# Optimization experiments

Measured on AMD Instinct MI355X. Metric: run time of the kernel, lower is better.

## Reference

```python
import jax, jax.numpy as jnp
import numpy as np

D_MODEL = 1024
D_STATE = 16
D_CONV = 4
EXPAND = 2
D_INNER = D_MODEL * EXPAND


def setup_inputs() -> dict:
    key = jax.random.key(0)
    ks = jax.random.split(key, 8)
    B, L = 2, 2048
    x = jax.random.normal(ks[0], (B, L, D_MODEL), dtype=jnp.float32)
    # in_proj: Linear(d_model -> 2*d_inner), no bias
    W_in = jax.random.normal(ks[1], (D_MODEL, 2 * D_INNER), dtype=jnp.float32) / np.sqrt(D_MODEL)
    # depthwise conv1d: (d_inner, 1, d_conv) + bias
    conv_w = jax.random.normal(ks[2], (D_INNER, 1, D_CONV), dtype=jnp.float32) / np.sqrt(D_CONV)
    conv_b = jax.random.normal(ks[3], (D_INNER,), dtype=jnp.float32) * 0.01
    # x_proj: Linear(d_inner -> 2*d_state + 1), no bias
    W_x = jax.random.normal(ks[4], (D_INNER, 2 * D_STATE + 1), dtype=jnp.float32) / np.sqrt(D_INNER)
    # A_log ~ Uniform(-log(d_state), -1)
    A_log = jax.random.uniform(ks[5], (D_INNER, D_STATE), dtype=jnp.float32,
                               minval=-np.log(D_STATE), maxval=-1.0)
    D_param = jnp.ones((D_INNER,), dtype=jnp.float32)
    W_out = jax.random.normal(ks[6], (D_INNER, D_MODEL), dtype=jnp.float32) / np.sqrt(D_INNER)
    return {"x": x, "W_in": W_in, "conv_w": conv_w, "conv_b": conv_b,
            "W_x": W_x, "A_log": A_log, "D_param": D_param, "W_out": W_out}


def _selective_scan(x, delta, A, Bm, Cm):
    # x:(B,L,D), delta:(B,L), A:(D,N), Bm/Cm:(B,L,N)
    Bsz, L, Dd = x.shape
    N = A.shape[1]
    h0 = jnp.zeros((Bsz, Dd, N), dtype=x.dtype)

    def step(h, inp):
        dt, Bt, Ct, xt = inp  # (B,), wait dt:(B,), Bt:(B,N), Ct:(B,N), xt:(B,D)
        A_bar = jnp.exp(dt[:, None, None] * A)          # (B,D,N)
        dB = (dt[:, None] * Bt)[:, None, :]             # (B,1,N)
        h = A_bar * h + dB * xt[:, :, None]             # (B,D,N)
        y = jnp.einsum('bn,bdn->bd', Ct, h)             # (B,D)
        return h, y

    xs = (jnp.swapaxes(delta, 0, 1), jnp.swapaxes(Bm, 0, 1),
          jnp.swapaxes(Cm, 0, 1), jnp.swapaxes(x, 0, 1))
    _, ys = jax.lax.scan(step, h0, xs)                  # ys: (L,B,D)
    return jnp.swapaxes(ys, 0, 1)


def reference(x, W_in, conv_w, conv_b, W_x, A_log, D_param, W_out):
    B, L, _ = x.shape
    xr = x @ W_in                                       # (B,L,2*Di)
    x_inner, res = jnp.split(xr, 2, axis=-1)
    # causal depthwise conv: left-pad d_conv-1, valid conv == torch slice [:L]
    xc = jnp.swapaxes(x_inner, 1, 2)                    # (B,Di,L)
    xc = jax.lax.conv_general_dilated(
        xc, conv_w, window_strides=(1,), padding=[(D_CONV - 1, 0)],
        dimension_numbers=('NCH', 'OIH', 'NCH'), feature_group_count=D_INNER)
    xc = xc + conv_b[None, :, None]
    xc = jnp.swapaxes(xc, 1, 2)                         # (B,L,Di)
    xc = jax.nn.silu(xc)
    ssm_params = xc @ W_x                               # (B,L,1+2N)
    delta = jax.nn.softplus(ssm_params[..., 0])         # (B,L)
    Bm = ssm_params[..., 1:1 + D_STATE]                 # (B,L,N)
    Cm = ssm_params[..., 1 + D_STATE:]                  # (B,L,N)
    A = -jnp.exp(A_log)                                 # (Di,N)
    y = _selective_scan(xc, delta, A, Bm, Cm)           # (B,L,Di)
    y = y + xc * D_param[None, None, :]
    y = y * jax.nn.silu(res)
    return y @ W_out                                    # (B,L,d_model)
```

## Files before the change

kernel.cpp:

```cpp
#include <hip/hip_runtime.h>

#define L_SEQ 2048
#define NB    2
#define DMOD  1024
#define DIN   2048
#define NST   16
#define NROWS (NB*L_SEQ)
#define CL    64
#define NC    (L_SEQ/CL)

typedef unsigned short u16;
typedef _Float16 half8 __attribute__((ext_vector_type(8)));
typedef float f32x4 __attribute__((ext_vector_type(4)));
typedef short short8 __attribute__((ext_vector_type(8)));

__device__ __forceinline__ float siluf(float v){ return v / (1.f + __expf(-v)); }
__device__ __forceinline__ u16 f2h_bits(float v){ _Float16 h = (_Float16)v; return __builtin_bit_cast(u16, h); }
__device__ __forceinline__ float h2f(u16 v){ return (float)__builtin_bit_cast(_Float16, v); }
__device__ __forceinline__ float fexp2(float x){
#if __has_builtin(__builtin_amdgcn_exp2f)
    return __builtin_amdgcn_exp2f(x);
#else
    return __expf(x * 0.69314718056f);
#endif
}

__device__ __forceinline__ void gload16(const u16* g, u16* l)
{
    __builtin_amdgcn_global_load_lds(
        (const __attribute__((address_space(1))) void*)g,
        (__attribute__((address_space(3))) void*)l,
        16, 0, 0);
}

#define BARRIER() do { asm volatile("" ::: "memory"); __builtin_amdgcn_s_barrier(); asm volatile("" ::: "memory"); } while (0)
#define VMCNT2()  asm volatile("s_waitcnt vmcnt(2)" ::: "memory")

__global__ __launch_bounds__(256)
void prep_inputs(const float* __restrict__ x, const float* __restrict__ W_in,
                 const float* __restrict__ W_out, const float* __restrict__ Wx,
                 u16* __restrict__ x16, u16* __restrict__ Bt1,
                 u16* __restrict__ Bt3, u16* __restrict__ WxT16)
{
    __shared__ float s[64][65];
    const int bid = blockIdx.x, tid = threadIdx.x;
    if (bid < 4096) {
        int i = bid * 256 + tid;
        float4 v = ((const float4*)x)[i];
        ushort4 o;
        o.x = f2h_bits(v.x); o.y = f2h_bits(v.y); o.z = f2h_bits(v.z); o.w = f2h_bits(v.w);
        *(ushort4*)&x16[(size_t)i * 4] = o;
    } else if (bid < 5632) {
        const float* in; u16* outT; int R, C, rblk, cblk;
        if (bid < 5120) { int b = bid - 4096; in = W_in;  outT = Bt1; R = 1024; C = 4096; cblk = b & 63; rblk = b >> 6; }
        else            { int b = bid - 5120; in = W_out; outT = Bt3; R = 2048; C = 1024; cblk = b & 15; rblk = b >> 4; }
        int r0 = rblk * 64, c0 = cblk * 64;
        int tc = tid & 63, ty = tid >> 6;
        #pragma unroll
        for (int j = 0; j < 16; j++) {
            int r = ty + j * 4;
            s[r][tc] = in[(size_t)(r0 + r) * C + c0 + tc];
        }
        __syncthreads();
        #pragma unroll
        for (int j = 0; j < 16; j++) {
            int nn = ty + j * 4;
            outT[(size_t)(c0 + nn) * R + r0 + tc] = f2h_bits(s[tc][nn]);
        }
    } else {
        int idx = (bid - 5632) * 256 + tid;
        int n = idx >> 11, k = idx & 2047;
        float v = (n < 33) ? Wx[k * 33 + n] : 0.f;
        WxT16[idx] = f2h_bits(v);
    }
}

template<int EPI>
__global__ __launch_bounds__(512, 2)
void gemm8(const u16* __restrict__ A, const u16* __restrict__ Bt,
           void* __restrict__ C0v, void* __restrict__ C1v,
           int M, int N, int KLEN, int lda, int ldb)
{
    __shared__ __align__(16) u16 As[2 * 256 * 64];
    __shared__ __align__(16) u16 Bs[2 * 256 * 64];
    const int tid  = threadIdx.x;
    const int lane = tid & 63;
    const int w    = tid >> 6;
    const int wm   = w >> 2, wn = w & 3;
    const int bm = blockIdx.y * 256, bn = blockIdx.x * 256;
    const int kBase = blockIdx.z * KLEN;

    const int srow8 = lane >> 3;
    const int sunit = (lane & 7) ^ srow8;
    const u16* Ag = A  + (size_t)(bm + srow8) * lda + kBase + sunit * 8;
    const u16* Bg = Bt + (size_t)(bn + srow8) * ldb + kBase + sunit * 8;
    const int rw = w * 16;

    const int fr  = lane & 15;
    const int sl0 = ((lane >> 4) ^ (fr & 7)) * 8;
    int aOffs[8], bOffs[4];
    #pragma unroll
    for (int mi = 0; mi < 8; mi++) aOffs[mi] = (wm * 128 + mi * 16 + fr) * 64 + sl0;
    #pragma unroll
    for (int ni = 0; ni < 4; ni++) bOffs[ni] = (ni * 64 + wn * 16 + fr) * 64 + sl0;

    f32x4 acc[8][4];
    #pragma unroll
    for (int i = 0; i < 8; i++)
        #pragma unroll
        for (int j = 0; j < 4; j++)
            acc[i][j] = (f32x4){0.f, 0.f, 0.f, 0.f};

    auto stage2 = [&](const u16* G, int ld, int rbase, int kcol, u16* ldsDst) {
        gload16(G + (size_t)rbase * ld + kcol, ldsDst);
        gload16(G + (size_t)(rbase + 8) * ld + kcol, ldsDst + 8 * 64);
    };

    const int NT = KLEN >> 6;
    stage2(Ag, lda, 0 + rw, 0, &As[(0 + rw) * 64]);
    stage2(Ag, lda, 128 + rw, 0, &As[(128 + rw) * 64]);
    stage2(Bg, ldb, 0 + rw, 0, &Bs[(0 + rw) * 64]);
    stage2(Bg, ldb, 128 + rw, 0, &Bs[(128 + rw) * 64]);
    VMCNT2();
    BARRIER();

    for (int t = 0; t < NT; ++t) {
        const int cO = (t & 1) << 14;
        const int nO = cO ^ 16384;
        const int kn = (t + 1) << 6;
        const bool pf = (t + 1) < NT;
        half8 af[8], bf0, bf1;

        #pragma unroll
        for (int mi = 0; mi < 8; mi++) af[mi] = *(const half8*)&As[cO + aOffs[mi]];
        bf0 = *(const half8*)&Bs[cO + bOffs[0]];
        bf1 = *(const half8*)&Bs[cO + bOffs[1]];
        if (pf) stage2(Ag, lda, 0 + rw, kn, &As[nO + (0 + rw) * 64]);
        BARRIER();
        __builtin_amdgcn_s_setprio(1);
        #pragma unroll
        for (int mi = 0; mi < 8; mi++) acc[mi][0] = __builtin_amdgcn_mfma_f32_16x16x32_f16(af[mi], bf0, acc[mi][0], 0, 0, 0);
        #pragma unroll
        for (int mi = 0; mi < 8; mi++) acc[mi][1] = __builtin_amdgcn_mfma_f32_16x16x32_f16(af[mi], bf1, acc[mi][1], 0, 0, 0);
        __builtin_amdgcn_s_setprio(0);
        VMCNT2();
        BARRIER();

        bf0 = *(const half8*)&Bs[cO + bOffs[2]];
        bf1 = *(const half8*)&Bs[cO + bOffs[3]];
        if (pf) stage2(Ag, lda, 128 + rw, kn, &As[nO + (128 + rw) * 64]);
        BARRIER();
        __builtin_amdgcn_s_setprio(1);
        #pragma unroll
        for (int mi = 0; mi < 8; mi++) acc[mi][2] = __builtin_amdgcn_mfma_f32_16x16x32_f16(af[mi], bf0, acc[mi][2], 0, 0, 0);
        #pragma unroll
        for (int mi = 0; mi < 8; mi++) acc[mi][3] = __builtin_amdgcn_mfma_f32_16x16x32_f16(af[mi], bf1, acc[mi][3], 0, 0, 0);
        __builtin_amdgcn_s_setprio(0);
        BARRIER();

        #pragma unroll
        for (int mi = 0; mi < 8; mi++) af[mi] = *(const half8*)&As[cO + (aOffs[mi] ^ 32)];
        bf0 = *(const half8*)&Bs[cO + (bOffs[0] ^ 32)];
        bf1 = *(const half8*)&Bs[cO + (bOffs[1] ^ 32)];
        if (pf) stage2(Bg, ldb, 0 + rw, kn, &Bs[nO + (0 + rw) * 64]);
        BARRIER();
        __builtin_amdgcn_s_setprio(1);
        #pragma unroll
        for (int mi = 0; mi < 8; mi++) acc[mi][0] = __builtin_amdgcn_mfma_f32_16x16x32_f16(af[mi], bf0, acc[mi][0], 0, 0, 0);
        #pragma unroll
        for (int mi = 0; mi < 8; mi++) acc[mi][1] = __builtin_amdgcn_mfma_f32_16x16x32_f16(af[mi], bf1, acc[mi][1], 0, 0, 0);
        __builtin_amdgcn_s_setprio(0);
        BARRIER();

        bf0 = *(const half8*)&Bs[cO + (bOffs[2] ^ 32)];
        bf1 = *(const half8*)&Bs[cO + (bOffs[3] ^ 32)];
        if (pf) stage2(Bg, ldb, 128 + rw, kn, &Bs[nO + (128 + rw) * 64]);
        BARRIER();
        __builtin_amdgcn_s_setprio(1);
        #pragma unroll
        for (int mi = 0; mi < 8; mi++) acc[mi][2] = __builtin_amdgcn_mfma_f32_16x16x32_f16(af[mi], bf0, acc[mi][2], 0, 0, 0);
        #pragma unroll
        for (int mi = 0; mi < 8; mi++) acc[mi][3] = __builtin_amdgcn_mfma_f32_16x16x32_f16(af[mi], bf1, acc[mi][3], 0, 0, 0);
        __builtin_amdgcn_s_setprio(0);
        VMCNT2();
        BARRIER();
    }

    const int cr = (lane >> 4) * 4;
    #pragma unroll
    for (int mi = 0; mi < 8; mi++) {
        #pragma unroll
        for (int ni = 0; ni < 4; ni++) {
            #pragma unroll
            for (int q = 0; q < 4; q++) {
                int row = bm + wm * 128 + mi * 16 + cr + q;
                int col = bn + ni * 64 + wn * 16 + fr;
                float v = acc[mi][ni][q];
                if (EPI == 1) {
                    int half = N >> 1;
                    if (col < half) ((u16*)C0v)[(size_t)row * half + col] = f2h_bits(v);
                    else            ((u16*)C1v)[(size_t)row * half + col - half] = f2h_bits(siluf(v));
                } else {
                    ((u16*)C0v)[((size_t)blockIdx.z * M + row) * N + col] = f2h_bits(v);
                }
            }
        }
    }
}

__global__ __launch_bounds__(256)
void add_partials4(const u16* __restrict__ p, float* __restrict__ out)
{
    int i = blockIdx.x * 256 + threadIdx.x;
    const size_t stride = (size_t)NROWS * DMOD;
    float acc[8] = {0,0,0,0,0,0,0,0};
    #pragma unroll
    for (int z = 0; z < 4; z++) {
        short8 a = *(const short8*)&p[z * stride + (size_t)i * 8];
        #pragma unroll
        for (int j = 0; j < 8; j++) acc[j] += h2f((u16)a[j]);
    }
    float4 o0 = {acc[0], acc[1], acc[2], acc[3]};
    float4 o1 = {acc[4], acc[5], acc[6], acc[7]};
    *(float4*)&out[(size_t)i * 8]     = o0;
    *(float4*)&out[(size_t)i * 8 + 4] = o1;
}

__global__ __launch_bounds__(256)
void conv_silu16(const u16* __restrict__ xin16, const float* __restrict__ cw,
                 const float* __restrict__ cb, u16* __restrict__ xc16)
{
    int idx = blockIdx.x * 256 + threadIdx.x;
    int d8 = idx & 255;
    int t  = (idx >> 8) & (L_SEQ - 1);
    int b  = idx >> 19;
    int d  = d8 << 3;
    const float4* cw4 = (const float4*)cw;
    float4 w[8];
    #pragma unroll
    for (int j = 0; j < 8; j++) w[j] = cw4[d + j];
    float acc[8];
    {
        float4 b0 = *(const float4*)&cb[d];
        float4 b1 = *(const float4*)&cb[d + 4];
        acc[0]=b0.x; acc[1]=b0.y; acc[2]=b0.z; acc[3]=b0.w;
        acc[4]=b1.x; acc[5]=b1.y; acc[6]=b1.z; acc[7]=b1.w;
    }
    #pragma unroll
    for (int k = 0; k < 4; k++) {
        int tt = t + k - 3;
        if (tt >= 0) {
            short8 v = *(const short8*)&xin16[((size_t)(b * L_SEQ + tt)) * DIN + d];
            #pragma unroll
            for (int j = 0; j < 8; j++)
                acc[j] = fmaf(h2f((u16)v[j]), (&w[j].x)[k], acc[j]);
        }
    }
    short8 o;
    #pragma unroll
    for (int j = 0; j < 8; j++) o[j] = (short)f2h_bits(siluf(acc[j]));
    *(short8*)&xc16[(size_t)idx * 8] = o;
}

__global__ __launch_bounds__(256)
void gemm2_mfma(const u16* __restrict__ A, const u16* __restrict__ Bt, float* __restrict__ pb)
{
    __shared__ __align__(16) u16 As[64 * 64];
    __shared__ __align__(16) u16 Bs[48 * 64];
    const int tid = threadIdx.x, lane = tid & 63, w = tid >> 6;
    const int bm = blockIdx.x * 64;
    const int kz = blockIdx.y;
    const int arow = tid >> 2;
    const int au   = (tid & 3) << 1;
    f32x4 acc[3];
    acc[0] = acc[1] = acc[2] = (f32x4){0.f, 0.f, 0.f, 0.f};

    for (int it = 0; it < 4; ++it) {
        const int k0 = kz * 256 + it * 64;
        short8 ra0 = *(const short8*)&A[(size_t)(bm + arow) * DIN + k0 + au * 8];
        short8 ra1 = *(const short8*)&A[(size_t)(bm + arow) * DIN + k0 + (au + 1) * 8];
        short8 rb0, rb1;
        if (tid < 192) {
            rb0 = *(const short8*)&Bt[(size_t)arow * DIN + k0 + au * 8];
            rb1 = *(const short8*)&Bt[(size_t)arow * DIN + k0 + (au + 1) * 8];
        }
        __syncthreads();
        {
            int s0 = au ^ (arow & 7), s1 = (au + 1) ^ (arow & 7);
            *(short8*)&As[arow * 64 + s0 * 8] = ra0;
            *(short8*)&As[arow * 64 + s1 * 8] = ra1;
            if (tid < 192) {
                *(short8*)&Bs[arow * 64 + s0 * 8] = rb0;
                *(short8*)&Bs[arow * 64 + s1 * 8] = rb1;
            }
        }
        __syncthreads();
        #pragma unroll
        for (int kk = 0; kk < 2; kk++) {
            int r = w * 16 + (lane & 15);
            int sl = (kk * 4 + (lane >> 4)) ^ (r & 7);
            half8 af = *(const half8*)&As[r * 64 + sl * 8];
            #pragma unroll
            for (int ni = 0; ni < 3; ni++) {
                int br = ni * 16 + (lane & 15);
                int bsl = (kk * 4 + (lane >> 4)) ^ (br & 7);
                half8 bf = *(const half8*)&Bs[br * 64 + bsl * 8];
                acc[ni] = __builtin_amdgcn_mfma_f32_16x16x32_f16(af, bf, acc[ni], 0, 0, 0);
            }
        }
    }
    #pragma unroll
    for (int ni = 0; ni < 3; ni++) {
        #pragma unroll
        for (int q = 0; q < 4; q++) {
            int row = bm + w * 16 + (lane >> 4) * 4 + q;
            int col = ni * 16 + (lane & 15);
            pb[((size_t)kz * NROWS + row) * 48 + col] = acc[ni][q];
        }
    }
}

__global__ __launch_bounds__(256)
void gemm2_reduce(const float* __restrict__ pb, float* __restrict__ delta,
                  float* __restrict__ Bm, float* __restrict__ Cm)
{
    int idx = blockIdx.x * 256 + threadIdx.x;
    int row = idx / 48, col = idx - row * 48;
    float s = 0.f;
    #pragma unroll
    for (int kz = 0; kz < 8; kz++) s += pb[(size_t)kz * NROWS * 48 + idx];
    if (col == 0)       delta[row] = fmaxf(s, 0.f) + log1pf(__expf(-fabsf(s)));
    else if (col < 17)  Bm[row * NST + col - 1]  = s;
    else if (col < 33)  Cm[row * NST + col - 17] = s;
}

__global__ __launch_bounds__(256)
void scan_part1_reg(const u16* __restrict__ xc16, const float* __restrict__ delta,
                    const float* __restrict__ Bm, const float* __restrict__ A_log,
                    float* __restrict__ h_loc, float* __restrict__ Pc)
{
    const int b = blockIdx.z, c = blockIdx.y;
    const int d = blockIdx.x * 256 + threadIdx.x;
    float ka[16];
    {
        const float4* Av = (const float4*)(A_log + (size_t)d * 16);
        #pragma unroll
        for (int q = 0; q < 4; q++) {
            float4 a = Av[q];
            ka[q*4+0] = -__expf(a.x) * 1.44269504f;
            ka[q*4+1] = -__expf(a.y) * 1.44269504f;
            ka[q*4+2] = -__expf(a.z) * 1.44269504f;
            ka[q*4+3] = -__expf(a.w) * 1.44269504f;
        }
    }
    float h[16];
    #pragma unroll
    for (int n = 0; n < 16; n++) h[n] = 0.f;
    float S = 0.f;
    const int rowbase = b * L_SEQ + c * CL;
    #pragma unroll 2
    for (int t = 0; t < CL; ++t) {
        const int rowg = rowbase + t;
        const float dt = delta[rowg];
        const float4* Bv = (const float4*)(Bm + (size_t)rowg * 16);
        float4 b0 = Bv[0], b1 = Bv[1], b2 = Bv[2], b3 = Bv[3];
        float bb[16] = {b0.x,b0.y,b0.z,b0.w, b1.x,b1.y,b1.z,b1.w,
                        b2.x,b2.y,b2.z,b2.w, b3.x,b3.y,b3.z,b3.w};
        const float xt = h2f(xc16[(size_t)rowg * DIN + d]);
        const float dtx = dt * xt;
        S += dt;
        #pragma unroll
        for (int n = 0; n < 16; n++) {
            float a = fexp2(dt * ka[n]);
            h[n] = fmaf(a, h[n], bb[n] * dtx);
        }
    }
    float* hp = h_loc + (((size_t)(b * NC + c) * DIN) + d) * 16;
    float* pp = Pc    + (((size_t)(b * NC + c) * DIN) + d) * 16;
    #pragma unroll
    for (int q = 0; q < 4; q++) {
        *(float4*)&hp[q*4] = (float4){h[q*4+0], h[q*4+1], h[q*4+2], h[q*4+3]};
        *(float4*)&pp[q*4] = (float4){fexp2(S*ka[q*4+0]), fexp2(S*ka[q*4+1]),
                                      fexp2(S*ka[q*4+2]), fexp2(S*ka[q*4+3])};
    }
}

__global__ __launch_bounds__(256)
void scan_carry(const float* __restrict__ h_loc, const float* __restrict__ Pc,
                float* __restrict__ H_in)
{
    int gid = blockIdx.x * 256 + threadIdx.x;
    int b = gid >> 15, r = gid & 32767;
    float H = 0.f;
    for (int c = 0; c < NC; ++c) {
        size_t idx = ((size_t)(b * NC + c) << 15) + r;
        H_in[idx] = H;
        H = fmaf(Pc[idx], H, h_loc[idx]);
    }
}

__global__ __launch_bounds__(256)
void scan_part3_reg(const u16* __restrict__ xc16, const float* __restrict__ delta,
                    const float* __restrict__ Bm, const float* __restrict__ Cm,
                    const float* __restrict__ A_log, const float* __restrict__ Dp,
                    const u16* __restrict__ res16, const float* __restrict__ H_in,
                    u16* __restrict__ yh)
{
    const int b = blockIdx.z, c = blockIdx.y;
    const int d = blockIdx.x * 256 + threadIdx.x;
    float ka[16];
    {
        const float4* Av = (const float4*)(A_log + (size_t)d * 16);
        #pragma unroll
        for (int q = 0; q < 4; q++) {
            float4 a = Av[q];
            ka[q*4+0] = -__expf(a.x) * 1.44269504f;
            ka[q*4+1] = -__expf(a.y) * 1.44269504f;
            ka[q*4+2] = -__expf(a.z) * 1.44269504f;
            ka[q*4+3] = -__expf(a.w) * 1.44269504f;
        }
    }
    float h[16];
    {
        const float4* Hv = (const float4*)(H_in + (((size_t)(b * NC + c) * DIN) + d) * 16);
        #pragma unroll
        for (int q = 0; q < 4; q++) {
            float4 v = Hv[q];
            h[q*4+0]=v.x; h[q*4+1]=v.y; h[q*4+2]=v.z; h[q*4+3]=v.w;
        }
    }
    const float Dpd = Dp[d];
    const int rowbase = b * L_SEQ + c * CL;
    #pragma unroll 2
    for (int t = 0; t < CL; ++t) {
        const int rowg = rowbase + t;
        const float dt = delta[rowg];
        const float4* Bv = (const float4*)(Bm + (size_t)rowg * 16);
        const float4* Cv = (const float4*)(Cm + (size_t)rowg * 16);
        float4 b0 = Bv[0], b1 = Bv[1], b2 = Bv[2], b3 = Bv[3];
        float4 c0 = Cv[0], c1 = Cv[1], c2 = Cv[2], c3 = Cv[3];
        float bb[16] = {b0.x,b0.y,b0.z,b0.w, b1.x,b1.y,b1.z,b1.w,
                        b2.x,b2.y,b2.z,b2.w, b3.x,b3.y,b3.z,b3.w};
        float cc[16] = {c0.x,c0.y,c0.z,c0.w, c1.x,c1.y,c1.z,c1.w,
                        c2.x,c2.y,c2.z,c2.w, c3.x,c3.y,c3.z,c3.w};
        const float xt = h2f(xc16[(size_t)rowg * DIN + d]);
        const float rt = h2f(res16[(size_t)rowg * DIN + d]);
        const float dtx = dt * xt;
        float y = 0.f;
        #pragma unroll
        for (int n = 0; n < 16; n++) {
            float a = fexp2(dt * ka[n]);
            h[n] = fmaf(a, h[n], bb[n] * dtx);
            y = fmaf(cc[n], h[n], y);
        }
        y = (y + xt * Dpd) * rt;
        yh[(size_t)rowg * DIN + d] = f2h_bits(y);
    }
}

extern "C" void kernel_launch(void* const* d_in, const int* in_sizes, int n_in,
                              void* d_out, int out_size, void* d_ws, size_t ws_size,
                              hipStream_t stream)
{
    const float* x     = (const float*)d_in[0];
    const float* W_in  = (const float*)d_in[1];
    const float* cw    = (const float*)d_in[2];
    const float* cb    = (const float*)d_in[3];
    const float* Wx    = (const float*)d_in[4];
    const float* A_log = (const float*)d_in[5];
    const float* Dp    = (const float*)d_in[6];
    const float* W_out = (const float*)d_in[7];
    float* out = (float*)d_out;
    float* ws  = (float*)d_ws;

    u16*   xin16 = (u16*)(ws);
    u16*   y16   = (u16*)(ws);
    u16*   res16 = (u16*)(ws + 4194304);
    u16*   xc16  = (u16*)(ws + 8388608);
    u16*   x16   = (u16*)(ws + 12582912);
    u16*   p4    = (u16*)(ws + 12582912);
    u16*   Bt1   = (u16*)(ws + 14680064);
    float* pb    = ws + 14680064;
    u16*   WxT16 = (u16*)(ws + 20971520);
    float* delta = ws + 21020672;
    float* Bm    = ws + 21024768;
    float* Cm    = ws + 21090304;
    float* h_loc = ws + 21155840;
    float* Pc    = ws + 23252992;
    float* H_in  = ws + 25350144;
    u16*   Bt3   = (u16*)(ws + 27447296);

    dim3 blk(256), blk512(512);

    prep_inputs<<<dim3(6016), blk, 0, stream>>>(x, W_in, W_out, Wx, x16, Bt1, Bt3, WxT16);
    gemm8<1><<<dim3(16, 16, 1), blk512, 0, stream>>>(x16, Bt1, xin16, res16,
                                                     NROWS, 2 * DIN, DMOD, DMOD, DMOD);
    conv_silu16<<<dim3(NB * L_SEQ * (DIN / 8) / 256), blk, 0, stream>>>(xin16, cw, cb, xc16);
    gemm2_mfma<<<dim3(NROWS / 64, 8), blk, 0, stream>>>(xc16, WxT16, pb);
    gemm2_reduce<<<dim3(NROWS * 48 / 256), blk, 0, stream>>>(pb, delta, Bm, Cm);
    scan_part1_reg<<<dim3(DIN / 256, NC, NB), blk, 0, stream>>>(xc16, delta, Bm, A_log, h_loc, Pc);
    scan_carry<<<dim3(NB * DIN * NST / 256), blk, 0, stream>>>(h_loc, Pc, H_in);
    scan_part3_reg<<<dim3(DIN / 256, NC, NB), blk, 0, stream>>>(xc16, delta, Bm, Cm, A_log, Dp, res16, H_in, y16);
    gemm8<2><<<dim3(DMOD / 256, NROWS / 256, 4), blk512, 0, stream>>>(y16, Bt3, p4, nullptr,
                                                                     NROWS, DMOD, DIN / 4, DIN, DIN);
    add_partials4<<<dim3(NROWS * DMOD / 8 / 256), blk, 0, stream>>>(p4, out);
}
```

Measured before the change: 207.3 us.

## Tile depthwise conv through shared memory and drop setprio in GEMM loop

```diff
diff --git a/kernel.cpp b/kernel.cpp
--- a/kernel.cpp
+++ b/kernel.cpp
@@ -137,12 +137,10 @@
         bf1 = *(const half8*)&Bs[cO + bOffs[1]];
         if (pf) stage2(Ag, lda, 0 + rw, kn, &As[nO + (0 + rw) * 64]);
         BARRIER();
-        __builtin_amdgcn_s_setprio(1);
         #pragma unroll
         for (int mi = 0; mi < 8; mi++) acc[mi][0] = __builtin_amdgcn_mfma_f32_16x16x32_f16(af[mi], bf0, acc[mi][0], 0, 0, 0);
         #pragma unroll
         for (int mi = 0; mi < 8; mi++) acc[mi][1] = __builtin_amdgcn_mfma_f32_16x16x32_f16(af[mi], bf1, acc[mi][1], 0, 0, 0);
-        __builtin_amdgcn_s_setprio(0);
         VMCNT2();
         BARRIER();
 
@@ -150,12 +148,10 @@
         bf1 = *(const half8*)&Bs[cO + bOffs[3]];
         if (pf) stage2(Ag, lda, 128 + rw, kn, &As[nO + (128 + rw) * 64]);
         BARRIER();
-        __builtin_amdgcn_s_setprio(1);
         #pragma unroll
         for (int mi = 0; mi < 8; mi++) acc[mi][2] = __builtin_amdgcn_mfma_f32_16x16x32_f16(af[mi], bf0, acc[mi][2], 0, 0, 0);
         #pragma unroll
         for (int mi = 0; mi < 8; mi++) acc[mi][3] = __builtin_amdgcn_mfma_f32_16x16x32_f16(af[mi], bf1, acc[mi][3], 0, 0, 0);
-        __builtin_amdgcn_s_setprio(0);
         BARRIER();
 
         #pragma unroll
@@ -164,24 +160,20 @@
         bf1 = *(const half8*)&Bs[cO + (bOffs[1] ^ 32)];
         if (pf) stage2(Bg, ldb, 0 + rw, kn, &Bs[nO + (0 + rw) * 64]);
         BARRIER();
-        __builtin_amdgcn_s_setprio(1);
         #pragma unroll
         for (int mi = 0; mi < 8; mi++) acc[mi][0] = __builtin_amdgcn_mfma_f32_16x16x32_f16(af[mi], bf0, acc[mi][0], 0, 0, 0);
         #pragma unroll
         for (int mi = 0; mi < 8; mi++) acc[mi][1] = __builtin_amdgcn_mfma_f32_16x16x32_f16(af[mi], bf1, acc[mi][1], 0, 0, 0);
-        __builtin_amdgcn_s_setprio(0);
         BARRIER();
 
         bf0 = *(const half8*)&Bs[cO + (bOffs[2] ^ 32)];
         bf1 = *(const half8*)&Bs[cO + (bOffs[3] ^ 32)];
         if (pf) stage2(Bg, ldb, 128 + rw, kn, &Bs[nO + (128 + rw) * 64]);
         BARRIER();
-        __builtin_amdgcn_s_setprio(1);
         #pragma unroll
         for (int mi = 0; mi < 8; mi++) acc[mi][2] = __builtin_amdgcn_mfma_f32_16x16x32_f16(af[mi], bf0, acc[mi][2], 0, 0, 0);
         #pragma unroll
         for (int mi = 0; mi < 8; mi++) acc[mi][3] = __builtin_amdgcn_mfma_f32_16x16x32_f16(af[mi], bf1, acc[mi][3], 0, 0, 0);
-        __builtin_amdgcn_s_setprio(0);
         VMCNT2();
         BARRIER();
     }
@@ -227,39 +219,52 @@
 }
 
 __global__ __launch_bounds__(256)
-void conv_silu16(const u16* __restrict__ xin16, const float* __restrict__ cw,
-                 const float* __restrict__ cb, u16* __restrict__ xc16)
-{
-    int idx = blockIdx.x * 256 + threadIdx.x;
-    int d8 = idx & 255;
-    int t  = (idx >> 8) & (L_SEQ - 1);
-    int b  = idx >> 19;
-    int d  = d8 << 3;
+void conv_silu16t(const u16* __restrict__ xin16, const float* __restrict__ cw,
+                  const float* __restrict__ cb, u16* __restrict__ xc16)
+{
+    __shared__ u16 sx[35][136];
+    const int d0 = blockIdx.x << 7, t0 = blockIdx.y << 5, b = blockIdx.z;
+    const int tid = threadIdx.x;
+    for (int i = tid; i < 35 * 16; i += 256) {
+        int r = i >> 4, u = i & 15;
+        int t = t0 - 3 + r;
+        short8 v = {0,0,0,0,0,0,0,0};
+        if (t >= 0) v = *(const short8*)&xin16[((size_t)(b * L_SEQ + t)) * DIN + d0 + u * 8];
+        *(short8*)&sx[r][u * 8] = v;
+    }
+    __syncthreads();
+    const int u  = tid & 15;
+    const int tl = tid >> 4;
+    const int d  = d0 + u * 8;
     const float4* cw4 = (const float4*)cw;
     float4 w[8];
     #pragma unroll
     for (int j = 0; j < 8; j++) w[j] = cw4[d + j];
-    float acc[8];
+    float bias[8];
     {
         float4 b0 = *(const float4*)&cb[d];
         float4 b1 = *(const float4*)&cb[d + 4];
-        acc[0]=b0.x; acc[1]=b0.y; acc[2]=b0.z; acc[3]=b0.w;
-        acc[4]=b1.x; acc[5]=b1.y; acc[6]=b1.z; acc[7]=b1.w;
-    }
-    #pragma unroll
-    for (int k = 0; k < 4; k++) {
-        int tt = t + k - 3;
-        if (tt >= 0) {
-            short8 v = *(const short8*)&xin16[((size_t)(b * L_SEQ + tt)) * DIN + d];
+        bias[0]=b0.x; bias[1]=b0.y; bias[2]=b0.z; bias[3]=b0.w;
+        bias[4]=b1.x; bias[5]=b1.y; bias[6]=b1.z; bias[7]=b1.w;
+    }
+    #pragma unroll
+    for (int half = 0; half < 2; half++) {
+        const int t_l = tl + half * 16;
+        float acc[8];
+        #pragma unroll
+        for (int j = 0; j < 8; j++) acc[j] = bias[j];
+        #pragma unroll
+        for (int k = 0; k < 4; k++) {
+            short8 v = *(const short8*)&sx[t_l + k][u * 8];
             #pragma unroll
             for (int j = 0; j < 8; j++)
                 acc[j] = fmaf(h2f((u16)v[j]), (&w[j].x)[k], acc[j]);
         }
-    }
-    short8 o;
-    #pragma unroll
-    for (int j = 0; j < 8; j++) o[j] = (short)f2h_bits(siluf(acc[j]));
-    *(short8*)&xc16[(size_t)idx * 8] = o;
+        short8 o;
+        #pragma unroll
+        for (int j = 0; j < 8; j++) o[j] = (short)f2h_bits(siluf(acc[j]));
+        *(short8*)&xc16[((size_t)(b * L_SEQ + t0 + t_l)) * DIN + d] = o;
+    }
 }
 
 __global__ __launch_bounds__(256)
@@ -495,7 +500,7 @@
     prep_inputs<<<dim3(6016), blk, 0, stream>>>(x, W_in, W_out, Wx, x16, Bt1, Bt3, WxT16);
     gemm8<1><<<dim3(16, 16, 1), blk512, 0, stream>>>(x16, Bt1, xin16, res16,
                                                      NROWS, 2 * DIN, DMOD, DMOD, DMOD);
-    conv_silu16<<<dim3(NB * L_SEQ * (DIN / 8) / 256), blk, 0, stream>>>(xin16, cw, cb, xc16);
+    conv_silu16t<<<dim3(DIN / 128, L_SEQ / 32, NB), blk, 0, stream>>>(xin16, cw, cb, xc16);
     gemm2_mfma<<<dim3(NROWS / 64, 8), blk, 0, stream>>>(xc16, WxT16, pb);
     gemm2_reduce<<<dim3(NROWS * 48 / 256), blk, 0, stream>>>(pb, delta, Bm, Cm);
     scan_part1_reg<<<dim3(DIN / 256, NC, NB), blk, 0, stream>>>(xc16, delta, Bm, A_log, h_loc, Pc);
```

New measurement: 188.2 us. -9.2%, faster.
